# Kernel tuning notes

Hardware: AMD Instinct MI355X
Metric: run time of the kernel (lower is better)

## Reference

```python
import jax, jax.numpy as jnp
import numpy as np


def _lstm_dir(x, w_ih, w_hh, b, reverse):
    # x: [B,T,I]; w_ih: [4H,I]; w_hh: [4H,H]; b: [4H] (b_ih+b_hh combined)
    B = x.shape[0]
    H = w_hh.shape[1]
    pre = jnp.einsum('bti,gi->btg', x, w_ih) + b  # [B,T,4H]
    if reverse:
        pre = pre[:, ::-1]
    def step(carry, g):
        h, c = carry
        g = g + h @ w_hh.T
        i, f, gg, o = jnp.split(g, 4, axis=-1)  # torch gate order i,f,g,o
        i = jax.nn.sigmoid(i)
        f = jax.nn.sigmoid(f)
        gg = jnp.tanh(gg)
        o = jax.nn.sigmoid(o)
        c = f * c + i * gg
        h = o * jnp.tanh(c)
        return (h, c), h
    h0 = jnp.zeros((B, H), x.dtype)
    _, hs = jax.lax.scan(step, (h0, h0), pre.transpose(1, 0, 2))
    hs = hs.transpose(1, 0, 2)  # [B,T,H]
    if reverse:
        hs = hs[:, ::-1]
    return hs


def _bilstm_layer(x, w_ih, w_hh, b):
    # w_ih: [2,4H,I] (dir 0 = fwd, dir 1 = bwd)
    fwd = _lstm_dir(x, w_ih[0], w_hh[0], b[0], False)
    bwd = _lstm_dir(x, w_ih[1], w_hh[1], b[1], True)
    return jnp.concatenate([fwd, bwd], axis=-1)  # [B,T,2H]


def setup_inputs() -> dict:
    key = jax.random.key(0)
    V, E, H = 50000, 128, 128   # vocab, token embed dim, per-direction hidden
    B, S, T = 32, 50, 40        # batch, sentences, tokens per sentence
    D = 2 * H                   # 256 = bi-LSTM output width
    ks = iter(jax.random.split(key, 32))
    def p(shape, scale=0.05):
        return (jax.random.normal(next(ks), shape, dtype=jnp.float32) * scale)
    inp = {
        'inputs': jax.random.randint(next(ks), (B, S, T), 0, V, dtype=jnp.int32),
        'emb': p((V, E)),
        # sentence encoder LSTM (2 layers, bidirectional)
        'enc_w_ih0': p((2, 4 * H, E)), 'enc_w_hh0': p((2, 4 * H, H)), 'enc_b0': p((2, 4 * H)),
        'enc_w_ih1': p((2, 4 * H, D)), 'enc_w_hh1': p((2, 4 * H, H)), 'enc_b1': p((2, 4 * H)),
        # document LSTM (2 layers, bidirectional)
        'doc_w_ih0': p((2, 4 * H, D)), 'doc_w_hh0': p((2, 4 * H, H)), 'doc_b0': p((2, 4 * H)),
        'doc_w_ih1': p((2, 4 * H, D)), 'doc_w_hh1': p((2, 4 * H, H)), 'doc_b1': p((2, 4 * H)),
        # linear heads
        'content_w': p((1, D)), 'content_b': p((1,)),
        'docl_w': p((D, D)), 'docl_b': p((D,)),
        'sal_w': p((D, D)), 'sal_b': p((D,)),
        'nov_w': p((D, D)), 'nov_b': p((D,)),
    }
    return inp


def reference(inputs, emb,
              enc_w_ih0, enc_w_hh0, enc_b0, enc_w_ih1, enc_w_hh1, enc_b1,
              doc_w_ih0, doc_w_hh0, doc_b0, doc_w_ih1, doc_w_hh1, doc_b1,
              content_w, content_b, docl_w, docl_b, sal_w, sal_b, nov_w, nov_b):
    B, S, T = inputs.shape
    # --- sentence encoder over all B*S sentences ---
    tok = emb[inputs.reshape(-1, T)]                     # [B*S, T, E]
    h = _bilstm_layer(tok, enc_w_ih0, enc_w_hh0, enc_b0)  # [B*S, T, 2H]
    h = _bilstm_layer(h, enc_w_ih1, enc_w_hh1, enc_b1)
    sent = jnp.mean(h, axis=1).reshape(B, S, -1)         # [B, S, 256]
    # --- document LSTM over sentences ---
    out = _bilstm_layer(sent, doc_w_ih0, doc_w_hh0, doc_b0)
    out = _bilstm_layer(out, doc_w_ih1, doc_w_hh1, doc_b1)  # [B, S, 256]
    doc_emb = jnp.tanh(jnp.mean(out, axis=1) @ docl_w.T + docl_b)  # [B, 256]
    content = (out @ content_w.T + content_b)[..., 0]    # [B, S]
    sal_vec = doc_emb @ sal_w.T + sal_b                  # [B, 256]
    salience = jnp.einsum('bsd,bd->bs', out, sal_vec)    # [B, S]
    pred = content + salience
    # --- novelty recurrence over sentences ---
    summary0 = jnp.zeros((B, out.shape[2]), out.dtype)
    def step(summary, i):
        nov_vec = jnp.tanh(summary) @ nov_w.T + nov_b    # [B, 256]
        nov = jnp.einsum('bsd,bd->bs', out, nov_vec)     # [B, S]
        prob = jax.nn.sigmoid(pred - nov)
        summary = summary + prob[:, i, None] * out[:, i, :]
        return summary, nov
    _, novs = jax.lax.scan(step, summary0, jnp.arange(S))
    novelty = novs[-1]
    return pred - novelty
```

## Files before the change

### kernel.cpp

```cpp
#include <hip/hip_runtime.h>
#include <hip/hip_bf16.h>
#include <math.h>


__device__ __forceinline__ float sigm(float x) { return 1.f / (1.f + expf(-x)); }

__global__ void transpose_k(const float* __restrict__ in, float* __restrict__ out,
                            int R, int C) {
    __shared__ float tile[32][33];
    int z = blockIdx.z;
    in += (size_t)z * R * C;
    out += (size_t)z * R * C;
    int bx = blockIdx.x * 32, by = blockIdx.y * 32;
    int tx = threadIdx.x, ty = threadIdx.y;
    #pragma unroll
    for (int j = 0; j < 32; j += 8) {
        tile[ty + j][tx] = in[(size_t)(by + ty + j) * C + bx + tx];
    }
    __syncthreads();
    #pragma unroll
    for (int j = 0; j < 32; j += 8) {
        out[(size_t)(bx + ty + j) * R + by + tx] = tile[tx][ty + j];
    }
}

__global__ void pack_w(const float* __restrict__ ih, const float* __restrict__ hh,
                       float* __restrict__ dst, int E) {
    int ROWS = E + 128;
    size_t total = (size_t)2 * ROWS * 512;
    for (size_t i = (size_t)blockIdx.x * 256 + threadIdx.x; i < total;
         i += (size_t)gridDim.x * 256) {
        int g = (int)(i & 3);
        int k = (int)((i >> 2) & 127);
        size_t rr = i >> 9;
        int r = (int)(rr % ROWS);
        int dir = (int)(rr / ROWS);
        float v = (r < E) ? ih[((size_t)dir * 512 + g * 128 + k) * E + r]
                          : hh[((size_t)dir * 512 + g * 128 + k) * 128 + (r - E)];
        dst[i] = v;
    }
}

__global__ void pack_bt(const float* __restrict__ ih, const float* __restrict__ b,
                        float* __restrict__ bt, float* __restrict__ bv, int E) {
    size_t total = (size_t)E * 1024;
    for (size_t i = (size_t)blockIdx.x * 256 + threadIdx.x; i < total;
         i += (size_t)gridDim.x * 256) {
        int c = (int)(i & 1023);
        int e = (int)(i >> 10);
        int dir = c >> 9;
        int gk = c & 511;
        bt[i] = ih[((size_t)dir * 512 + gk) * E + e];
        if (e == 0) bv[c] = b[dir * 512 + gk];
    }
}

template <int K, int GATHER>
__global__ __launch_bounds__(256, 4) void gemm_x(
    const float* __restrict__ A, const int* __restrict__ ids,
    const float* __restrict__ emb, const float* __restrict__ bt,
    const float* __restrict__ bv, float* __restrict__ C) {
    int n0 = blockIdx.x * 128;
    int c0 = blockIdx.y * 128;
    int tid = threadIdx.x;
    int tx = tid & 15, ty = tid >> 4;
    __shared__ float As[32][132];
    __shared__ float Bs[32][132];
    float acc[8][8];
    #pragma unroll
    for (int i = 0; i < 8; i++)
        #pragma unroll
        for (int j = 0; j < 8; j++) acc[i][j] = 0.f;

    for (int k0 = 0; k0 < K; k0 += 32) {
        #pragma unroll
        for (int it = 0; it < 4; it++) {
            int lin = tid + it * 256;
            int r = lin >> 3, kq = lin & 7;
            const float* src;
            if (GATHER) {
                src = emb + (size_t)ids[n0 + r] * 128;
            } else {
                src = A + (size_t)(n0 + r) * K;
            }
            float4 v = *(const float4*)&src[k0 + kq * 4];
            As[kq * 4 + 0][r] = v.x;
            As[kq * 4 + 1][r] = v.y;
            As[kq * 4 + 2][r] = v.z;
            As[kq * 4 + 3][r] = v.w;
        }
        #pragma unroll
        for (int it = 0; it < 4; it++) {
            int lin = tid + it * 256;
            int kk = lin >> 5, c4 = lin & 31;
            float4 v = *(const float4*)&bt[(size_t)(k0 + kk) * 1024 + c0 + c4 * 4];
            *(float4*)&Bs[kk][c4 * 4] = v;
        }
        __syncthreads();
        #pragma unroll 4
        for (int kk = 0; kk < 32; kk++) {
            float4 a0 = *(const float4*)&As[kk][ty * 8];
            float4 a1 = *(const float4*)&As[kk][ty * 8 + 4];
            float4 b0 = *(const float4*)&Bs[kk][tx * 8];
            float4 b1 = *(const float4*)&Bs[kk][tx * 8 + 4];
            const float av[8] = {a0.x, a0.y, a0.z, a0.w, a1.x, a1.y, a1.z, a1.w};
            const float bvv[8] = {b0.x, b0.y, b0.z, b0.w, b1.x, b1.y, b1.z, b1.w};
            #pragma unroll
            for (int i = 0; i < 8; i++)
                #pragma unroll
                for (int j = 0; j < 8; j++)
                    acc[i][j] = fmaf(av[i], bvv[j], acc[i][j]);
        }
        __syncthreads();
    }
    float bias8[8];
    #pragma unroll
    for (int j = 0; j < 8; j++) bias8[j] = bv[c0 + tx * 8 + j];
    #pragma unroll
    for (int i = 0; i < 8; i++) {
        int row = n0 + ty * 8 + i;
        float* cp = C + (size_t)row * 1024 + c0 + tx * 8;
        float4 r0 = make_float4(acc[i][0] + bias8[0], acc[i][1] + bias8[1],
                                acc[i][2] + bias8[2], acc[i][3] + bias8[3]);
        float4 r1 = make_float4(acc[i][4] + bias8[4], acc[i][5] + bias8[5],
                                acc[i][6] + bias8[6], acc[i][7] + bias8[7]);
        *(float4*)cp = r0;
        *(float4*)(cp + 4) = r1;
    }
}

template <int MODE>
__global__ __launch_bounds__(512) void word_scanH(
    const float* __restrict__ pre,
    const float* __restrict__ wph,
    float* __restrict__ outp) {
    const int T = 40;
    int wg = blockIdx.x;
    int dir = wg / 200;
    int grp = wg - dir * 200;
    int base = grp * 8;
    int tid = threadIdx.x;
    int k = tid & 127;
    int gp = (tid >> 7) & 1;
    int hf = tid >> 8;
    int sb = hf * 4;

    __shared__ float hs[128][12];
    __shared__ float pa[2][128][12];

    const float* wp = wph + (size_t)dir * 128 * 512 + k * 4 + gp * 2;

    float c[4], ms[4];
    #pragma unroll
    for (int j = 0; j < 4; j++) { c[j] = 0.f; ms[j] = 0.f; }

    for (int t = 0; t < T; t++) {
        int te = dir ? (T - 1 - t) : t;
        float a0[4], a1[4];
        #pragma unroll
        for (int j = 0; j < 4; j++) {
            size_t n = (size_t)(base + sb + j) * T + te;
            const float* pr = pre + n * 1024 + (size_t)dir * 512 + gp * 256 + k;
            a0[j] = pr[0];
            a1[j] = pr[128];
        }
        if (t > 0) {
            #pragma unroll 8
            for (int r = 0; r < 128; r++) {
                const float2 w = *(const float2*)(wp + (size_t)r * 512);
                const float4 x0 = *(const float4*)&hs[r][sb];
                const float xv[4] = {x0.x, x0.y, x0.z, x0.w};
                #pragma unroll
                for (int j = 0; j < 4; j++) {
                    a0[j] = fmaf(w.x, xv[j], a0[j]);
                    a1[j] = fmaf(w.y, xv[j], a1[j]);
                }
            }
        }
        if (gp == 1) {
            #pragma unroll
            for (int j = 0; j < 4; j++) {
                pa[0][k][sb + j] = a0[j];
                pa[1][k][sb + j] = a1[j];
            }
        }
        __syncthreads();
        if (gp == 0) {
            float hv[4];
            #pragma unroll
            for (int j = 0; j < 4; j++) {
                float iv = sigm(a0[j]);
                float fv = sigm(a1[j]);
                float gv = tanhf(pa[0][k][sb + j]);
                float ov = sigm(pa[1][k][sb + j]);
                c[j] = fv * c[j] + iv * gv;
                hv[j] = ov * tanhf(c[j]);
            }
            *(float4*)&hs[k][sb] = make_float4(hv[0], hv[1], hv[2], hv[3]);
            if (MODE == 0) {
                #pragma unroll
                for (int j = 0; j < 4; j++) {
                    outp[(((size_t)(base + sb + j)) * T + te) * 256 +
                         (size_t)dir * 128 + k] = hv[j];
                }
            } else {
                #pragma unroll
                for (int j = 0; j < 4; j++) ms[j] += hv[j];
            }
        }
        __syncthreads();
    }
    if (MODE == 1 && gp == 0) {
        #pragma unroll
        for (int j = 0; j < 4; j++) {
            outp[(size_t)(base + sb + j) * 256 + (size_t)dir * 128 + k] =
                ms[j] * (1.f / T);
        }
    }
}

template <int E, int MODE>
__global__ __launch_bounds__(512) void word_scan2(
    const int* __restrict__ ids, const float* __restrict__ emb,
    const float* __restrict__ xin,
    const float* __restrict__ wpk,
    const float* __restrict__ bias,
    float* __restrict__ outp) {
    const int T = 40;
    const int ROWS = E + 128;
    int wg = blockIdx.x;
    int dir = wg / 100;
    int grp = wg - dir * 100;
    int base = grp * 16;
    int tid = threadIdx.x;
    int k = tid & 127;
    int gp = (tid >> 7) & 1;
    int hf = tid >> 8;
    int sb = hf * 8;

    __shared__ float xs[E][20];
    __shared__ float hs[128][20];
    __shared__ float pa[2][128][17];

    const float* wp = wpk + (size_t)dir * ROWS * 512 + k * 4 + gp * 2;
    const float* bb = bias + dir * 512;
    float bi = bb[k], bf_ = bb[128 + k], bg = bb[256 + k], bo = bb[384 + k];

    float c[8], ms[8];
    #pragma unroll
    for (int j = 0; j < 8; j++) { c[j] = 0.f; ms[j] = 0.f; }

    for (int t = 0; t < T; t++) {
        int te = dir ? (T - 1 - t) : t;
        {
            const int NF4 = 16 * (E / 4);
            for (int idx = tid; idx < NF4; idx += 512) {
                int s = idx / (E / 4);
                int e4 = idx - s * (E / 4);
                int seq = base + s;
                float4 v;
                if (MODE == 0) {
                    int id = ids[(size_t)seq * T + te];
                    v = *(const float4*)&emb[(size_t)id * 128 + e4 * 4];
                } else {
                    v = *(const float4*)&xin[((size_t)seq * T + te) * 256 + e4 * 4];
                }
                xs[e4 * 4 + 0][s] = v.x;
                xs[e4 * 4 + 1][s] = v.y;
                xs[e4 * 4 + 2][s] = v.z;
                xs[e4 * 4 + 3][s] = v.w;
            }
        }
        __syncthreads();

        float a0[8], a1[8];
        #pragma unroll
        for (int j = 0; j < 8; j++) { a0[j] = 0.f; a1[j] = 0.f; }

        #pragma unroll 4
        for (int e = 0; e < E; e++) {
            const float2 w = *(const float2*)(wp + (size_t)e * 512);
            const float4 x0 = *(const float4*)&xs[e][sb];
            const float4 x1 = *(const float4*)&xs[e][sb + 4];
            const float xv[8] = {x0.x, x0.y, x0.z, x0.w, x1.x, x1.y, x1.z, x1.w};
            #pragma unroll
            for (int j = 0; j < 8; j++) {
                a0[j] = fmaf(w.x, xv[j], a0[j]);
                a1[j] = fmaf(w.y, xv[j], a1[j]);
            }
        }
        if (t > 0) {
            const float* wh = wp + (size_t)E * 512;
            #pragma unroll 4
            for (int r = 0; r < 128; r++) {
                const float2 w = *(const float2*)(wh + (size_t)r * 512);
                const float4 x0 = *(const float4*)&hs[r][sb];
                const float4 x1 = *(const float4*)&hs[r][sb + 4];
                const float xv[8] = {x0.x, x0.y, x0.z, x0.w, x1.x, x1.y, x1.z, x1.w};
                #pragma unroll
                for (int j = 0; j < 8; j++) {
                    a0[j] = fmaf(w.x, xv[j], a0[j]);
                    a1[j] = fmaf(w.y, xv[j], a1[j]);
                }
            }
        }

        if (gp == 1) {
            #pragma unroll
            for (int j = 0; j < 8; j++) {
                pa[0][k][sb + j] = a0[j];
                pa[1][k][sb + j] = a1[j];
            }
        }
        __syncthreads();
        if (gp == 0) {
            float hv[8];
            #pragma unroll
            for (int j = 0; j < 8; j++) {
                float iv = sigm(a0[j] + bi);
                float fv = sigm(a1[j] + bf_);
                float gv = tanhf(pa[0][k][sb + j] + bg);
                float ov = sigm(pa[1][k][sb + j] + bo);
                c[j] = fv * c[j] + iv * gv;
                hv[j] = ov * tanhf(c[j]);
            }
            *(float4*)&hs[k][sb] = make_float4(hv[0], hv[1], hv[2], hv[3]);
            *(float4*)&hs[k][sb + 4] = make_float4(hv[4], hv[5], hv[6], hv[7]);
            if (MODE == 0) {
                #pragma unroll
                for (int j = 0; j < 8; j++) {
                    outp[(((size_t)(base + sb + j)) * T + te) * 256 +
                         (size_t)dir * 128 + k] = hv[j];
                }
            } else {
                #pragma unroll
                for (int j = 0; j < 8; j++) ms[j] += hv[j];
            }
        }
        __syncthreads();
    }
    if (MODE == 1 && gp == 0) {
        #pragma unroll
        for (int j = 0; j < 8; j++) {
            outp[(size_t)(base + sb + j) * 256 + (size_t)dir * 128 + k] =
                ms[j] * (1.f / T);
        }
    }
}

__global__ __launch_bounds__(256) void gemm_pre(
    const float* __restrict__ A, const float* __restrict__ Bt,
    const float* __restrict__ bias, float* __restrict__ C) {
    int dir = blockIdx.z;
    const float* B = Bt + (size_t)dir * 256 * 512;
    float* Cp = C + (size_t)dir * 1600 * 512;
    const float* bb = bias + (size_t)dir * 512;
    int n0 = blockIdx.x * 64, g0 = blockIdx.y * 64;
    int tid = threadIdx.x;
    int tx = tid & 15, ty = tid >> 4;
    __shared__ float AsT[32][72];
    __shared__ float Bs[32][72];
    float acc[4][4];
    #pragma unroll
    for (int i = 0; i < 4; i++)
        #pragma unroll
        for (int j = 0; j < 4; j++) acc[i][j] = 0.f;

    for (int k0 = 0; k0 < 256; k0 += 32) {
        #pragma unroll
        for (int it = 0; it < 2; it++) {
            int idx = tid + it * 256;
            int n = idx & 63, e4 = idx >> 6;
            float4 v = *(const float4*)&A[(size_t)(n0 + n) * 256 + k0 + e4 * 4];
            AsT[e4 * 4 + 0][n] = v.x;
            AsT[e4 * 4 + 1][n] = v.y;
            AsT[e4 * 4 + 2][n] = v.z;
            AsT[e4 * 4 + 3][n] = v.w;
        }
        #pragma unroll
        for (int it = 0; it < 2; it++) {
            int idx = tid + it * 256;
            int g4 = idx & 15, e = idx >> 4;
            float4 v = *(const float4*)&B[(size_t)(k0 + e) * 512 + g0 + g4 * 4];
            *(float4*)&Bs[e][g4 * 4] = v;
        }
        __syncthreads();
        #pragma unroll 8
        for (int kk = 0; kk < 32; kk++) {
            float4 a = *(const float4*)&AsT[kk][ty * 4];
            float4 b = *(const float4*)&Bs[kk][tx * 4];
            const float av[4] = {a.x, a.y, a.z, a.w};
            const float bv[4] = {b.x, b.y, b.z, b.w};
            #pragma unroll
            for (int i = 0; i < 4; i++)
                #pragma unroll
                for (int j = 0; j < 4; j++)
                    acc[i][j] = fmaf(av[i], bv[j], acc[i][j]);
        }
        __syncthreads();
    }
    #pragma unroll
    for (int i = 0; i < 4; i++) {
        #pragma unroll
        for (int j = 0; j < 4; j++) {
            Cp[(size_t)(n0 + ty * 4 + i) * 512 + g0 + tx * 4 + j] =
                acc[i][j] + bb[g0 + tx * 4 + j];
        }
    }
}

__global__ __launch_bounds__(512) void doc_scan2(
    const float* __restrict__ pre,
    const float* __restrict__ whh,
    float* __restrict__ outp) {
    const int S = 50;
    int wg = blockIdx.x;
    int dir = wg >> 4;
    int b0 = (wg & 15) * 2;
    int g = threadIdx.x;
    int k = g & 127, su = g >> 7;
    __shared__ float hsd[2][128];
    __shared__ float paD[2][512];
    const float* W = whh + (size_t)dir * 128 * 512;
    const float* p0 = pre + ((size_t)dir * 1600 + (size_t)b0 * 50) * 512;
    float cst = 0.f;
    for (int t = 0; t < S; t++) {
        int te = dir ? (S - 1 - t) : t;
        float a0 = p0[(size_t)te * 512 + g];
        float a1 = p0[((size_t)(50 + te)) * 512 + g];
        if (t > 0) {
            #pragma unroll 8
            for (int r = 0; r < 128; r++) {
                float w = W[(size_t)r * 512 + g];
                a0 = fmaf(w, hsd[0][r], a0);
                a1 = fmaf(w, hsd[1][r], a1);
            }
        }
        paD[0][g] = a0;
        paD[1][g] = a1;
        __syncthreads();
        if (g < 256) {
            float pi = paD[su][k], pf = paD[su][128 + k];
            float pg = paD[su][256 + k], po = paD[su][384 + k];
            float iv = sigm(pi), fv = sigm(pf), gv = tanhf(pg), ov = sigm(po);
            cst = fv * cst + iv * gv;
            float hv = ov * tanhf(cst);
            hsd[su][k] = hv;
            outp[((size_t)(b0 + su) * 50 + te) * 256 + (size_t)dir * 128 + k] = hv;
        }
        __syncthreads();
    }
}

__global__ __launch_bounds__(256) void head_kernel(
    const float* __restrict__ outv, const float* __restrict__ content_w,
    const float* __restrict__ content_b, const float* __restrict__ doclT,
    const float* __restrict__ docl_b, const float* __restrict__ salT,
    const float* __restrict__ sal_b, const float* __restrict__ novT,
    const float* __restrict__ nov_b, float* __restrict__ outp) {
    const int S = 50, D = 256;
    int b = blockIdx.x;
    int tid = threadIdx.x;
    __shared__ float oL[50][257];
    __shared__ float mb[256];
    __shared__ float de[256];
    __shared__ float svec[256];
    __shared__ float nvec[256];
    __shared__ float tsum[256];
    __shared__ float predL[64];
    __shared__ float nvL[64];
    __shared__ float red[4][64];

    const float* ob = outv + (size_t)b * S * D;
    for (int i = tid; i < S * D; i += 256) {
        int s = i >> 8, d = i & 255;
        oL[s][d] = ob[i];
    }
    __syncthreads();
    {
        float m = 0;
        for (int s = 0; s < S; s++) m += oL[s][tid];
        mb[tid] = m * (1.f / S);
    }
    __syncthreads();
    {
        float acc = docl_b[tid];
        for (int d = 0; d < D; d++) acc = fmaf(doclT[d * 256 + tid], mb[d], acc);
        de[tid] = tanhf(acc);
    }
    __syncthreads();
    {
        float acc = sal_b[tid];
        for (int d = 0; d < D; d++) acc = fmaf(salT[d * 256 + tid], de[d], acc);
        svec[tid] = acc;
    }
    __syncthreads();
    {
        int s = tid & 63, pw = tid >> 6;
        float ca = 0, sa = 0;
        if (s < S) {
            for (int i = 0; i < 64; i++) {
                int d = pw * 64 + i;
                float ov = oL[s][d];
                ca = fmaf(ov, content_w[d], ca);
                sa = fmaf(ov, svec[d], sa);
            }
        }
        red[pw][s] = ca + sa;
    }
    __syncthreads();
    if (tid < S) {
        predL[tid] = content_b[0] + red[0][tid] + red[1][tid] + red[2][tid] + red[3][tid];
    }
    float summ = 0.f;
    __syncthreads();
    for (int it = 0; it < S; ++it) {
        tsum[tid] = tanhf(summ);
        __syncthreads();
        {
            float acc = nov_b[tid];
            for (int d = 0; d < D; d++) acc = fmaf(novT[d * 256 + tid], tsum[d], acc);
            nvec[tid] = acc;
        }
        __syncthreads();
        {
            int s = tid & 63, pw = tid >> 6;
            float na = 0;
            if (s < S) {
                for (int i = 0; i < 64; i++) {
                    int d = pw * 64 + i;
                    na = fmaf(oL[s][d], nvec[d], na);
                }
            }
            red[pw][s] = na;
        }
        __syncthreads();
        if (tid < S) nvL[tid] = red[0][tid] + red[1][tid] + red[2][tid] + red[3][tid];
        __syncthreads();
        float prob = sigm(predL[it] - nvL[it]);
        summ = fmaf(prob, oL[it][tid], summ);
        __syncthreads();
    }
    if (tid < S) outp[(size_t)b * S + tid] = predL[tid] - nvL[tid];
}

extern "C" void kernel_launch(void* const* d_in, const int* in_sizes, int n_in,
                              void* d_out, int out_size, void* d_ws, size_t ws_size,
                              hipStream_t stream) {
    const int* ids = (const int*)d_in[0];
    const float* emb = (const float*)d_in[1];
    const float* e_ih0 = (const float*)d_in[2];
    const float* e_hh0 = (const float*)d_in[3];
    const float* e_b0 = (const float*)d_in[4];
    const float* e_ih1 = (const float*)d_in[5];
    const float* e_hh1 = (const float*)d_in[6];
    const float* e_b1 = (const float*)d_in[7];
    const float* d_ih0 = (const float*)d_in[8];
    const float* d_hh0 = (const float*)d_in[9];
    const float* d_b0 = (const float*)d_in[10];
    const float* d_ih1 = (const float*)d_in[11];
    const float* d_hh1 = (const float*)d_in[12];
    const float* d_b1 = (const float*)d_in[13];
    const float* content_w = (const float*)d_in[14];
    const float* content_b = (const float*)d_in[15];
    const float* docl_w = (const float*)d_in[16];
    const float* docl_b = (const float*)d_in[17];
    const float* sal_w = (const float*)d_in[18];
    const float* sal_b = (const float*)d_in[19];
    const float* nov_w = (const float*)d_in[20];
    const float* nov_b = (const float*)d_in[21];
    float* outp = (float*)d_out;

    float* ws = (float*)d_ws;
    size_t off = 0;
    auto alloc = [&](size_t n) { float* p = ws + off; off += n; return p; };
    float* wpk0 = alloc((size_t)2 * 256 * 512);
    float* wpk1 = alloc((size_t)2 * 384 * 512);
    float* wph0 = alloc((size_t)2 * 128 * 512);
    float* wph1 = alloc((size_t)2 * 128 * 512);
    float* btw0 = alloc((size_t)128 * 1024);
    float* btw1 = alloc((size_t)256 * 1024);
    float* bv0 = alloc(1024);
    float* bv1 = alloc(1024);
    float* bT_d0 = alloc((size_t)2 * 256 * 512);
    float* whh_d0 = alloc((size_t)2 * 128 * 512);
    float* bT_d1 = alloc((size_t)2 * 256 * 512);
    float* whh_d1 = alloc((size_t)2 * 128 * 512);
    float* wT_docl = alloc((size_t)256 * 256);
    float* wT_sal = alloc((size_t)256 * 256);
    float* wT_nov = alloc((size_t)256 * 256);
    float* sent = alloc((size_t)1600 * 256);
    float* pre_d0 = alloc((size_t)2 * 1600 * 512);
    float* d0out = alloc((size_t)1600 * 256);
    float* pre_d1 = alloc((size_t)2 * 1600 * 512);
    float* dout = alloc((size_t)1600 * 256);
    float* h0out = alloc((size_t)64000 * 256);
    size_t need_fallback = off * 4;
    float* pre = alloc((size_t)64000 * 1024);
    size_t need_hoist = off * 4;
    (void)in_sizes; (void)n_in; (void)out_size; (void)need_fallback;

    bool hoist = ws_size >= need_hoist;

    dim3 tb(32, 8);
    transpose_k<<<dim3(256 / 32, 512 / 32, 2), tb, 0, stream>>>(d_ih0, bT_d0, 512, 256);
    transpose_k<<<dim3(128 / 32, 512 / 32, 2), tb, 0, stream>>>(d_hh0, whh_d0, 512, 128);
    transpose_k<<<dim3(256 / 32, 512 / 32, 2), tb, 0, stream>>>(d_ih1, bT_d1, 512, 256);
    transpose_k<<<dim3(128 / 32, 512 / 32, 2), tb, 0, stream>>>(d_hh1, whh_d1, 512, 128);
    transpose_k<<<dim3(256 / 32, 256 / 32, 1), tb, 0, stream>>>(docl_w, wT_docl, 256, 256);
    transpose_k<<<dim3(256 / 32, 256 / 32, 1), tb, 0, stream>>>(sal_w, wT_sal, 256, 256);
    transpose_k<<<dim3(256 / 32, 256 / 32, 1), tb, 0, stream>>>(nov_w, wT_nov, 256, 256);

    if (hoist) {
        pack_w<<<256, 256, 0, stream>>>(e_hh0, e_hh0, wph0, 0);
        pack_w<<<256, 256, 0, stream>>>(e_hh1, e_hh1, wph1, 0);
        pack_bt<<<256, 256, 0, stream>>>(e_ih0, e_b0, btw0, bv0, 128);
        pack_bt<<<512, 256, 0, stream>>>(e_ih1, e_b1, btw1, bv1, 256);

        gemm_x<128, 1><<<dim3(500, 8), 256, 0, stream>>>(nullptr, ids, emb,
                                                         btw0, bv0, pre);
        word_scanH<0><<<400, 512, 0, stream>>>(pre, wph0, h0out);
        gemm_x<256, 0><<<dim3(500, 8), 256, 0, stream>>>(h0out, nullptr, nullptr,
                                                         btw1, bv1, pre);
        word_scanH<1><<<400, 512, 0, stream>>>(pre, wph1, sent);
    } else {
        pack_w<<<1024, 256, 0, stream>>>(e_ih0, e_hh0, wpk0, 128);
        pack_w<<<1536, 256, 0, stream>>>(e_ih1, e_hh1, wpk1, 256);
        word_scan2<128, 0><<<200, 512, 0, stream>>>(ids, emb, nullptr, wpk0, e_b0, h0out);
        word_scan2<256, 1><<<200, 512, 0, stream>>>(nullptr, nullptr, h0out, wpk1,
                                                    e_b1, sent);
    }

    gemm_pre<<<dim3(25, 8, 2), 256, 0, stream>>>(sent, bT_d0, d_b0, pre_d0);
    doc_scan2<<<32, 512, 0, stream>>>(pre_d0, whh_d0, d0out);
    gemm_pre<<<dim3(25, 8, 2), 256, 0, stream>>>(d0out, bT_d1, d_b1, pre_d1);
    doc_scan2<<<32, 512, 0, stream>>>(pre_d1, whh_d1, dout);

    head_kernel<<<32, 256, 0, stream>>>(dout, content_w, content_b, wT_docl, docl_b,
                                        wT_sal, sal_b, wT_nov, nov_b, outp);
}
```

Before: 2.501 ms.

## Repack LSTM weights two rows per float4 and chunk the hoisted word scan

Recurrent and input weights are repacked so that each thread loads one float4 holding two consecutive rows for both of its gates. This halves the global weight load instructions in the word-level scans. The hoisted path gains a middle tier that processes the 1600 sequences in two chunks with half the pre-activation buffer, using fewer sequences per workgroup. The fallback fused scan now runs 400 workgroups of 8 sequences instead of 200 of 16, and the bias is folded into the accumulator initialisation. With the default (large) workspace the main path runs as before, but with the new weight layout.

```diff
diff --git a/kernel.cpp b/kernel.cpp
--- a/kernel.cpp
+++ b/kernel.cpp
@@ -24,19 +24,22 @@
     }
 }
 
-__global__ void pack_w(const float* __restrict__ ih, const float* __restrict__ hh,
-                       float* __restrict__ dst, int E) {
-    int ROWS = E + 128;
-    size_t total = (size_t)2 * ROWS * 512;
+__global__ void pack_w4(const float* __restrict__ ih, const float* __restrict__ hh,
+                        float* __restrict__ dst, int E) {
+    int ROWS2 = (E + 128) >> 1;
+    size_t total = (size_t)2 * ROWS2 * 128 * 8;
     for (size_t i = (size_t)blockIdx.x * 256 + threadIdx.x; i < total;
          i += (size_t)gridDim.x * 256) {
-        int g = (int)(i & 3);
-        int k = (int)((i >> 2) & 127);
-        size_t rr = i >> 9;
-        int r = (int)(rr % ROWS);
-        int dir = (int)(rr / ROWS);
-        float v = (r < E) ? ih[((size_t)dir * 512 + g * 128 + k) * E + r]
-                          : hh[((size_t)dir * 512 + g * 128 + k) * 128 + (r - E)];
+        int f = (int)(i & 3);
+        int gp = (int)((i >> 2) & 1);
+        int k = (int)((i >> 3) & 127);
+        size_t rr = i >> 10;
+        int r2 = (int)(rr % ROWS2);
+        int dir = (int)(rr / ROWS2);
+        int row = r2 * 2 + (f >> 1);
+        int gate = gp * 2 + (f & 1);
+        float v = (row < E) ? ih[((size_t)dir * 512 + gate * 128 + k) * E + row]
+                            : hh[((size_t)dir * 512 + gate * 128 + k) * 128 + (row - E)];
         dst[i] = v;
     }
 }
@@ -129,12 +132,121 @@
     }
 }
 
-template <int MODE>
-__global__ __launch_bounds__(512) void word_scanH(
+template <int MODE, int SJ>
+__global__ __launch_bounds__(512) void word_scanH2(
     const float* __restrict__ pre,
-    const float* __restrict__ wph,
+    const float* __restrict__ wph4,
+    float* __restrict__ outp, int seqBase) {
+    const int T = 40;
+    const int HSTR = 3 * SJ;
+    const int PSTR = 2 * SJ + 1;
+    int wg = blockIdx.x;
+    int dir = wg / 200;
+    int grp = wg - dir * 200;
+    int lbase = grp * (2 * SJ);
+    int tid = threadIdx.x;
+    int k = tid & 127;
+    int gp = (tid >> 7) & 1;
+    int hf = tid >> 8;
+    int sb = hf * SJ;
+
+    __shared__ float hs[128][HSTR];
+    __shared__ float pa[2][128][PSTR];
+
+    const float* wq = wph4 + ((size_t)dir * 64 * 128 + k) * 8 + gp * 4;
+
+    float c[SJ], ms[SJ];
+    #pragma unroll
+    for (int j = 0; j < SJ; j++) { c[j] = 0.f; ms[j] = 0.f; }
+
+    for (int t = 0; t < T; t++) {
+        int te = dir ? (T - 1 - t) : t;
+        float a0[SJ], a1[SJ];
+        #pragma unroll
+        for (int j = 0; j < SJ; j++) {
+            size_t n = (size_t)(lbase + sb + j) * T + te;
+            const float* pr = pre + n * 1024 + (size_t)dir * 512 + gp * 256 + k;
+            a0[j] = pr[0];
+            a1[j] = pr[128];
+        }
+        if (t > 0) {
+            #pragma unroll 8
+            for (int r2 = 0; r2 < 64; r2++) {
+                float4 w = *(const float4*)(wq + (size_t)r2 * 1024);
+                float xv0[SJ], xv1[SJ];
+                if (SJ == 4) {
+                    float4 t0 = *(const float4*)&hs[2 * r2][sb];
+                    float4 t1 = *(const float4*)&hs[2 * r2 + 1][sb];
+                    xv0[0] = t0.x; xv0[1] = t0.y; xv0[2] = t0.z; xv0[3] = t0.w;
+                    xv1[0] = t1.x; xv1[1] = t1.y; xv1[2] = t1.z; xv1[3] = t1.w;
+                } else {
+                    float2 t0 = *(const float2*)&hs[2 * r2][sb];
+                    float2 t1 = *(const float2*)&hs[2 * r2 + 1][sb];
+                    xv0[0] = t0.x; xv0[1] = t0.y;
+                    xv1[0] = t1.x; xv1[1] = t1.y;
+                }
+                #pragma unroll
+                for (int j = 0; j < SJ; j++) {
+                    a0[j] = fmaf(w.x, xv0[j], fmaf(w.z, xv1[j], a0[j]));
+                    a1[j] = fmaf(w.y, xv0[j], fmaf(w.w, xv1[j], a1[j]));
+                }
+            }
+        }
+        if (gp == 1) {
+            #pragma unroll
+            for (int j = 0; j < SJ; j++) {
+                pa[0][k][sb + j] = a0[j];
+                pa[1][k][sb + j] = a1[j];
+            }
+        }
+        __syncthreads();
+        if (gp == 0) {
+            float hv[SJ];
+            #pragma unroll
+            for (int j = 0; j < SJ; j++) {
+                float iv = sigm(a0[j]);
+                float fv = sigm(a1[j]);
+                float gv = tanhf(pa[0][k][sb + j]);
+                float ov = sigm(pa[1][k][sb + j]);
+                c[j] = fv * c[j] + iv * gv;
+                hv[j] = ov * tanhf(c[j]);
+            }
+            if (SJ == 4) {
+                *(float4*)&hs[k][sb] = make_float4(hv[0], hv[1], hv[2], hv[3]);
+            } else {
+                *(float2*)&hs[k][sb] = make_float2(hv[0], hv[1]);
+            }
+            if (MODE == 0) {
+                #pragma unroll
+                for (int j = 0; j < SJ; j++) {
+                    outp[(((size_t)(seqBase + lbase + sb + j)) * T + te) * 256 +
+                         (size_t)dir * 128 + k] = hv[j];
+                }
+            } else {
+                #pragma unroll
+                for (int j = 0; j < SJ; j++) ms[j] += hv[j];
+            }
+        }
+        __syncthreads();
+    }
+    if (MODE == 1 && gp == 0) {
+        #pragma unroll
+        for (int j = 0; j < SJ; j++) {
+            outp[(size_t)(seqBase + lbase + sb + j) * 256 + (size_t)dir * 128 + k] =
+                ms[j] * (1.f / T);
+        }
+    }
+}
+
+template <int E, int MODE>
+__global__ __launch_bounds__(512) void word_fused(
+    const int* __restrict__ ids, const float* __restrict__ emb,
+    const float* __restrict__ xin,
+    const float* __restrict__ wpk4,
+    const float* __restrict__ bias,
     float* __restrict__ outp) {
     const int T = 40;
+    const int ROWS2 = (E + 128) / 2;
     int wg = blockIdx.x;
     int dir = wg / 200;
     int grp = wg - dir * 200;
@@ -145,115 +257,23 @@
     int hf = tid >> 8;
     int sb = hf * 4;
 
+    __shared__ float xs[E][12];
     __shared__ float hs[128][12];
-    __shared__ float pa[2][128][12];
-
-    const float* wp = wph + (size_t)dir * 128 * 512 + k * 4 + gp * 2;
+    __shared__ float pa[2][128][9];
+
+    const float* wq = wpk4 + ((size_t)dir * ROWS2 * 128 + k) * 8 + gp * 4;
+    const float* bb = bias + dir * 512;
+    float bA = bb[gp * 256 + k];
+    float bB = bb[gp * 256 + 128 + k];
 
     float c[4], ms[4];
     #pragma unroll
     for (int j = 0; j < 4; j++) { c[j] = 0.f; ms[j] = 0.f; }
-
-    for (int t = 0; t < T; t++) {
-        int te = dir ? (T - 1 - t) : t;
-        float a0[4], a1[4];
-        #pragma unroll
-        for (int j = 0; j < 4; j++) {
-            size_t n = (size_t)(base + sb + j) * T + te;
-            const float* pr = pre + n * 1024 + (size_t)dir * 512 + gp * 256 + k;
-            a0[j] = pr[0];
-            a1[j] = pr[128];
-        }
-        if (t > 0) {
-            #pragma unroll 8
-            for (int r = 0; r < 128; r++) {
-                const float2 w = *(const float2*)(wp + (size_t)r * 512);
-                const float4 x0 = *(const float4*)&hs[r][sb];
-                const float xv[4] = {x0.x, x0.y, x0.z, x0.w};
-                #pragma unroll
-                for (int j = 0; j < 4; j++) {
-                    a0[j] = fmaf(w.x, xv[j], a0[j]);
-                    a1[j] = fmaf(w.y, xv[j], a1[j]);
-                }
-            }
-        }
-        if (gp == 1) {
-            #pragma unroll
-            for (int j = 0; j < 4; j++) {
-                pa[0][k][sb + j] = a0[j];
-                pa[1][k][sb + j] = a1[j];
-            }
-        }
-        __syncthreads();
-        if (gp == 0) {
-            float hv[4];
-            #pragma unroll
-            for (int j = 0; j < 4; j++) {
-                float iv = sigm(a0[j]);
-                float fv = sigm(a1[j]);
-                float gv = tanhf(pa[0][k][sb + j]);
-                float ov = sigm(pa[1][k][sb + j]);
-                c[j] = fv * c[j] + iv * gv;
-                hv[j] = ov * tanhf(c[j]);
-            }
-            *(float4*)&hs[k][sb] = make_float4(hv[0], hv[1], hv[2], hv[3]);
-            if (MODE == 0) {
-                #pragma unroll
-                for (int j = 0; j < 4; j++) {
-                    outp[(((size_t)(base + sb + j)) * T + te) * 256 +
-                         (size_t)dir * 128 + k] = hv[j];
-                }
-            } else {
-                #pragma unroll
-                for (int j = 0; j < 4; j++) ms[j] += hv[j];
-            }
-        }
-        __syncthreads();
-    }
-    if (MODE == 1 && gp == 0) {
-        #pragma unroll
-        for (int j = 0; j < 4; j++) {
-            outp[(size_t)(base + sb + j) * 256 + (size_t)dir * 128 + k] =
-                ms[j] * (1.f / T);
-        }
-    }
-}
-
-template <int E, int MODE>
-__global__ __launch_bounds__(512) void word_scan2(
-    const int* __restrict__ ids, const float* __restrict__ emb,
-    const float* __restrict__ xin,
-    const float* __restrict__ wpk,
-    const float* __restrict__ bias,
-    float* __restrict__ outp) {
-    const int T = 40;
-    const int ROWS = E + 128;
-    int wg = blockIdx.x;
-    int dir = wg / 100;
-    int grp = wg - dir * 100;
-    int base = grp * 16;
-    int tid = threadIdx.x;
-    int k = tid & 127;
-    int gp = (tid >> 7) & 1;
-    int hf = tid >> 8;
-    int sb = hf * 8;
-
-    __shared__ float xs[E][20];
-    __shared__ float hs[128][20];
-    __shared__ float pa[2][128][17];
-
-    const float* wp = wpk + (size_t)dir * ROWS * 512 + k * 4 + gp * 2;
-    const float* bb = bias + dir * 512;
-    float bi = bb[k], bf_ = bb[128 + k], bg = bb[256 + k], bo = bb[384 + k];
-
-    float c[8], ms[8];
-    #pragma unroll
-    for (int j = 0; j < 8; j++) { c[j] = 0.f; ms[j] = 0.f; }
 
     for (int t = 0; t < T; t++) {
         int te = dir ? (T - 1 - t) : t;
         {
-            const int NF4 = 16 * (E / 4);
+            const int NF4 = 8 * (E / 4);
             for (int idx = tid; idx < NF4; idx += 512) {
                 int s = idx / (E / 4);
                 int e4 = idx - s * (E / 4);
@@ -273,75 +293,75 @@
         }
         __syncthreads();
 
-        float a0[8], a1[8];
-        #pragma unroll
-        for (int j = 0; j < 8; j++) { a0[j] = 0.f; a1[j] = 0.f; }
+        float a0[4] = {bA, bA, bA, bA};
+        float a1[4] = {bB, bB, bB, bB};
 
         #pragma unroll 4
-        for (int e = 0; e < E; e++) {
-            const float2 w = *(const float2*)(wp + (size_t)e * 512);
-            const float4 x0 = *(const float4*)&xs[e][sb];
-            const float4 x1 = *(const float4*)&xs[e][sb + 4];
-            const float xv[8] = {x0.x, x0.y, x0.z, x0.w, x1.x, x1.y, x1.z, x1.w};
+        for (int r2 = 0; r2 < E / 2; r2++) {
+            float4 w = *(const float4*)(wq + (size_t)r2 * 1024);
+            float4 t0 = *(const float4*)&xs[2 * r2][sb];
+            float4 t1 = *(const float4*)&xs[2 * r2 + 1][sb];
+            const float xv0[4] = {t0.x, t0.y, t0.z, t0.w};
+            const float xv1[4] = {t1.x, t1.y, t1.z, t1.w};
             #pragma unroll
-            for (int j = 0; j < 8; j++) {
-                a0[j] = fmaf(w.x, xv[j], a0[j]);
-                a1[j] = fmaf(w.y, xv[j], a1[j]);
+            for (int j = 0; j < 4; j++) {
+                a0[j] = fmaf(w.x, xv0[j], fmaf(w.z, xv1[j], a0[j]));
+                a1[j] = fmaf(w.y, xv0[j], fmaf(w.w, xv1[j], a1[j]));
             }
         }
         if (t > 0) {
-            const float* wh = wp + (size_t)E * 512;
+            const float* wh = wq + (size_t)(E / 2) * 1024;
             #pragma unroll 4
-            for (int r = 0; r < 128; r++) {
-                const float2 w = *(const float2*)(wh + (size_t)r * 512);
-                const float4 x0 = *(const float4*)&hs[r][sb];
-                const float4 x1 = *(const float4*)&hs[r][sb + 4];
-                const float xv[8] = {x0.x, x0.y, x0.z, x0.w, x1.x, x1.y, x1.z, x1.w};
-                #pragma unroll
-                for (int j = 0; j < 8; j++) {
-                    a0[j] = fmaf(w.x, xv[j], a0[j]);
-                    a1[j] = fmaf(w.y, xv[j], a1[j]);
+            for (int r2 = 0; r2 < 64; r2++) {
+                float4 w = *(const float4*)(wh + (size_t)r2 * 1024);
+                float4 t0 = *(const float4*)&hs[2 * r2][sb];
+                float4 t1 = *(const float4*)&hs[2 * r2 + 1][sb];
+                const float xv0[4] = {t0.x, t0.y, t0.z, t0.w};
+                const float xv1[4] = {t1.x, t1.y, t1.z, t1.w};
+                #pragma unroll
+                for (int j = 0; j < 4; j++) {
+                    a0[j] = fmaf(w.x, xv0[j], fmaf(w.z, xv1[j], a0[j]));
+                    a1[j] = fmaf(w.y, xv0[j], fmaf(w.w, xv1[j], a1[j]));
                 }
             }
         }
 
         if (gp == 1) {
             #pragma unroll
-            for (int j = 0; j < 8; j++) {
+            for (int j = 0; j < 4; j++) {
                 pa[0][k][sb + j] = a0[j];
                 pa[1][k][sb + j] = a1[j];
             }
         }
         __syncthreads();
         if (gp == 0) {
-            float hv[8];
+            float hv[4];
             #pragma unroll
-            for (int j = 0; j < 8; j++) {
-                float iv = sigm(a0[j] + bi);
-                float fv = sigm(a1[j] + bf_);
-                float gv = tanhf(pa[0][k][sb + j] + bg);
-                float ov = sigm(pa[1][k][sb + j] + bo);
+            for (int j = 0; j < 4; j++) {
+                float iv = sigm(a0[j]);
+                float fv = sigm(a1[j]);
+                float gv = tanhf(pa[0][k][sb + j]);
+                float ov = sigm(pa[1][k][sb + j]);
                 c[j] = fv * c[j] + iv * gv;
                 hv[j] = ov * tanhf(c[j]);
             }
             *(float4*)&hs[k][sb] = make_float4(hv[0], hv[1], hv[2], hv[3]);
-            *(float4*)&hs[k][sb + 4] = make_float4(hv[4], hv[5], hv[6], hv[7]);
             if (MODE == 0) {
                 #pragma unroll
-                for (int j = 0; j < 8; j++) {
+                for (int j = 0; j < 4; j++) {
                     outp[(((size_t)(base + sb + j)) * T + te) * 256 +
                          (size_t)dir * 128 + k] = hv[j];
                 }
             } else {
                 #pragma unroll
-                for (int j = 0; j < 8; j++) ms[j] += hv[j];
+                for (int j = 0; j < 4; j++) ms[j] += hv[j];
             }
         }
         __syncthreads();
     }
     if (MODE == 1 && gp == 0) {
         #pragma unroll
-        for (int j = 0; j < 8; j++) {
+        for (int j = 0; j < 4; j++) {
             outp[(size_t)(base + sb + j) * 256 + (size_t)dir * 128 + k] =
                 ms[j] * (1.f / T);
         }
@@ -574,10 +594,10 @@
     float* ws = (float*)d_ws;
     size_t off = 0;
     auto alloc = [&](size_t n) { float* p = ws + off; off += n; return p; };
-    float* wpk0 = alloc((size_t)2 * 256 * 512);
-    float* wpk1 = alloc((size_t)2 * 384 * 512);
-    float* wph0 = alloc((size_t)2 * 128 * 512);
-    float* wph1 = alloc((size_t)2 * 128 * 512);
+    float* wpk4_0 = alloc((size_t)2 * 256 * 512);
+    float* wpk4_1 = alloc((size_t)2 * 384 * 512);
+    float* wph4_0 = alloc((size_t)2 * 128 * 512);
+    float* wph4_1 = alloc((size_t)2 * 128 * 512);
     float* btw0 = alloc((size_t)128 * 1024);
     float* btw1 = alloc((size_t)256 * 1024);
     float* bv0 = alloc(1024);
@@ -595,12 +615,13 @@
     float* pre_d1 = alloc((size_t)2 * 1600 * 512);
     float* dout = alloc((size_t)1600 * 256);
     float* h0out = alloc((size_t)64000 * 256);
-    size_t need_fallback = off * 4;
-    float* pre = alloc((size_t)64000 * 1024);
-    size_t need_hoist = off * 4;
-    (void)in_sizes; (void)n_in; (void)out_size; (void)need_fallback;
-
-    bool hoist = ws_size >= need_hoist;
+    size_t base = off;
+    size_t needA = (base + (size_t)64000 * 1024) * 4;
+    size_t needB = (base + (size_t)32000 * 1024) * 4;
+    float* pre = ws + base;
+    (void)in_sizes; (void)n_in; (void)out_size;
+
+    int tier = (ws_size >= needA) ? 2 : (ws_size >= needB) ? 1 : 0;
 
     dim3 tb(32, 8);
     transpose_k<<<dim3(256 / 32, 512 / 32, 2), tb, 0, stream>>>(d_ih0, bT_d0, 512, 256);
@@ -611,23 +632,36 @@
     transpose_k<<<dim3(256 / 32, 256 / 32, 1), tb, 0, stream>>>(sal_w, wT_sal, 256, 256);
     transpose_k<<<dim3(256 / 32, 256 / 32, 1), tb, 0, stream>>>(nov_w, wT_nov, 256, 256);
 
-    if (hoist) {
-        pack_w<<<256, 256, 0, stream>>>(e_hh0, e_hh0, wph0, 0);
-        pack_w<<<256, 256, 0, stream>>>(e_hh1, e_hh1, wph1, 0);
+    if (tier > 0) {
+        pack_w4<<<256, 256, 0, stream>>>(e_hh0, e_hh0, wph4_0, 0);
+        pack_w4<<<256, 256, 0, stream>>>(e_hh1, e_hh1, wph4_1, 0);
         pack_bt<<<256, 256, 0, stream>>>(e_ih0, e_b0, btw0, bv0, 128);
         pack_bt<<<512, 256, 0, stream>>>(e_ih1, e_b1, btw1, bv1, 256);
 
-        gemm_x<128, 1><<<dim3(500, 8), 256, 0, stream>>>(nullptr, ids, emb,
-                                                         btw0, bv0, pre);
-        word_scanH<0><<<400, 512, 0, stream>>>(pre, wph0, h0out);
-        gemm_x<256, 0><<<dim3(500, 8), 256, 0, stream>>>(h0out, nullptr, nullptr,
-                                                         btw1, bv1, pre);
-        word_scanH<1><<<400, 512, 0, stream>>>(pre, wph1, sent);
+        int CS = (tier == 2) ? 1600 : 800;
+        int nch = 1600 / CS;
+        for (int c = 0; c < nch; ++c) {
+            gemm_x<128, 1><<<dim3(CS * 40 / 128, 8), 256, 0, stream>>>(
+                nullptr, ids + (size_t)c * CS * 40, emb, btw0, bv0, pre);
+            if (tier == 2)
+                word_scanH2<0, 4><<<400, 512, 0, stream>>>(pre, wph4_0, h0out, c * CS);
+            else
+                word_scanH2<0, 2><<<400, 512, 0, stream>>>(pre, wph4_0, h0out, c * CS);
+        }
+        for (int c = 0; c < nch; ++c) {
+            gemm_x<256, 0><<<dim3(CS * 40 / 128, 8), 256, 0, stream>>>(
+                h0out + (size_t)c * CS * 40 * 256, nullptr, nullptr, btw1, bv1, pre);
+            if (tier == 2)
+                word_scanH2<1, 4><<<400, 512, 0, stream>>>(pre, wph4_1, sent, c * CS);
+            else
+                word_scanH2<1, 2><<<400, 512, 0, stream>>>(pre, wph4_1, sent, c * CS);
+        }
     } else {
-        pack_w<<<1024, 256, 0, stream>>>(e_ih0, e_hh0, wpk0, 128);
-        pack_w<<<1536, 256, 0, stream>>>(e_ih1, e_hh1, wpk1, 256);
-        word_scan2<128, 0><<<200, 512, 0, stream>>>(ids, emb, nullptr, wpk0, e_b0, h0out);
-        word_scan2<256, 1><<<200, 512, 0, stream>>>(nullptr, nullptr, h0out, wpk1,
+        pack_w4<<<512, 256, 0, stream>>>(e_ih0, e_hh0, wpk4_0, 128);
+        pack_w4<<<768, 256, 0, stream>>>(e_ih1, e_hh1, wpk4_1, 256);
+        word_fused<128, 0><<<400, 512, 0, stream>>>(ids, emb, nullptr, wpk4_0,
+                                                    e_b0, h0out);
+        word_fused<256, 1><<<400, 512, 0, stream>>>(nullptr, nullptr, h0out, wpk4_1,
                                                     e_b1, sent);
     }
 
```

After: 3.148 ms. +25.9%, slower.
